# Optimization experiments

Hardware: AMD Instinct MI355X
Metric: run time of the kernel (lower is better)

## Reference

```python
import jax, jax.numpy as jnp
import numpy as np

N, E, F, H, C = 50000, 800000, 602, 32, 41
BN_EPS = 1e-5


def _mlp(h, Wa, ba, Wb, bb):
    return jax.nn.relu(h @ Wa + ba) @ Wb + bb


def _bn(h, gamma, beta):
    # BatchNorm1d training mode: per-feature batch mean / biased variance
    m = jnp.mean(h, axis=0)
    v = jnp.var(h, axis=0)
    return (h - m) * jax.lax.rsqrt(v + BN_EPS) * gamma + beta


def _gin(x, row, col, Wa, ba, Wb, bb):
    # sum-aggregate neighbor features (SpMM via gather + segment_sum), eps=0
    agg = jax.ops.segment_sum(x[col], row, num_segments=x.shape[0])
    return _mlp(x + agg, Wa, ba, Wb, bb)


def setup_inputs() -> dict:
    key = jax.random.key(0)
    ks = jax.random.split(key, 16)
    s = 0.05
    inp = {
        "x": jax.random.normal(ks[0], (N, F), dtype=jnp.float32),
        "row": jax.random.randint(ks[1], (E,), 0, N),
        "col": jax.random.randint(ks[2], (E,), 0, N),
        # conv1 MLP
        "W1a": jax.random.normal(ks[3], (F, H), dtype=jnp.float32) * s,
        "b1a": jnp.zeros((H,), jnp.float32),
        "W1b": jax.random.normal(ks[4], (H, H), dtype=jnp.float32) * s,
        "b1b": jnp.zeros((H,), jnp.float32),
        "g1": jnp.ones((H,), jnp.float32),
        "be1": jnp.zeros((H,), jnp.float32),
        # conv2 MLP
        "W2a": jax.random.normal(ks[5], (H, H), dtype=jnp.float32) * s,
        "b2a": jnp.zeros((H,), jnp.float32),
        "W2b": jax.random.normal(ks[6], (H, H), dtype=jnp.float32) * s,
        "b2b": jnp.zeros((H,), jnp.float32),
        "g2": jnp.ones((H,), jnp.float32),
        "be2": jnp.zeros((H,), jnp.float32),
        # heads
        "Wf1": jax.random.normal(ks[7], (H, H), dtype=jnp.float32) * s,
        "bf1": jnp.zeros((H,), jnp.float32),
        "Wf2": jax.random.normal(ks[8], (H, C), dtype=jnp.float32) * s,
        "bf2": jnp.zeros((C,), jnp.float32),
    }
    return inp


def reference(x, row, col, W1a, b1a, W1b, b1b, g1, be1,
              W2a, b2a, W2b, b2b, g2, be2, Wf1, bf1, Wf2, bf2):
    h = _bn(_gin(x, row, col, W1a, b1a, W1b, b1b), g1, be1)
    h = _bn(_gin(h, row, col, W2a, b2a, W2b, b2b), g2, be2)
    h = jax.nn.relu(h @ Wf1 + bf1)
    return h @ Wf2 + bf2
```

## Files before the change

### kernel.cpp

```cpp
#include <hip/hip_runtime.h>
#include <hip/hip_bf16.h>

#define N_NODES 50000
#define F_IN    602
#define H_DIM   32
#define C_OUT   41
#define E_EDGES 800000
#define BN_EPS  1e-5f

__global__ __launch_bounds__(256) void k_gemm_in_v3(
    const float* __restrict__ x, const float* __restrict__ W,
    float* __restrict__ p) {
  __shared__ float xs[64 * 68];
  __shared__ float ws[32 * 68];
  const int tid = threadIdx.x;
  const int r0 = blockIdx.x * 64;

  const int cg  = tid & 15;
  const int rgg = tid >> 4;

  const int srow = tid >> 5;
  const int fe   = tid & 31;

  const float* xrp[8];
  #pragma unroll
  for (int pp = 0; pp < 8; pp++) {
    int rr = r0 + pp * 8 + srow;
    if (rr > N_NODES - 1) rr = N_NODES - 1;
    xrp[pp] = x + (size_t)rr * F_IN;
  }

  float2 xr[8];
  float4 wr[2];

  #pragma unroll
  for (int pp = 0; pp < 8; pp++)
    xr[pp] = *(const float2*)(xrp[pp] + 2 * fe);
  #pragma unroll
  for (int q = 0; q < 2; q++)
    wr[q] = *(const float4*)(W + q * 1024 + 4 * tid);

  float acc[4][2] = {};

  for (int ch = 0; ch < 10; ch++) {
    __syncthreads();
    #pragma unroll
    for (int pp = 0; pp < 8; pp++)
      *(float2*)&xs[(pp * 8 + srow) * 68 + 2 * fe] = xr[pp];
    #pragma unroll
    for (int q = 0; q < 2; q++) {
      int off = q * 1024 + 4 * tid;
      int kk = off >> 5, c0 = off & 31;
      ws[(c0 + 0) * 68 + kk] = wr[q].x;
      ws[(c0 + 1) * 68 + kk] = wr[q].y;
      ws[(c0 + 2) * 68 + kk] = wr[q].z;
      ws[(c0 + 3) * 68 + kk] = wr[q].w;
    }
    __syncthreads();
    if (ch < 9) {
      const int k0 = (ch + 1) * 64;
      #pragma unroll
      for (int pp = 0; pp < 8; pp++) {
        int k = k0 + 2 * fe;
        float2 v = {0.f, 0.f};
        if (k + 2 <= F_IN) v = *(const float2*)(xrp[pp] + k);
        xr[pp] = v;
      }
      #pragma unroll
      for (int q = 0; q < 2; q++) {
        int off = k0 * H_DIM + q * 1024 + 4 * tid;
        float4 v = {0.f, 0.f, 0.f, 0.f};
        if (off < F_IN * H_DIM) v = *(const float4*)(W + off);
        wr[q] = v;
      }
    }
    #pragma unroll
    for (int kq = 0; kq < 16; kq++) {
      float4 xv[4], wv[2];
      #pragma unroll
      for (int i = 0; i < 4; i++) xv[i] = *(float4*)&xs[(rgg + 16 * i) * 68 + kq * 4];
      #pragma unroll
      for (int j = 0; j < 2; j++) wv[j] = *(float4*)&ws[(cg + 16 * j) * 68 + kq * 4];
      #pragma unroll
      for (int i = 0; i < 4; i++)
        #pragma unroll
        for (int j = 0; j < 2; j++)
          acc[i][j] += xv[i].x * wv[j].x + xv[i].y * wv[j].y +
                       xv[i].z * wv[j].z + xv[i].w * wv[j].w;
    }
  }

  #pragma unroll
  for (int i = 0; i < 4; i++) {
    int gr = r0 + rgg + 16 * i;
    if (gr < N_NODES) {
      #pragma unroll
      for (int j = 0; j < 2; j++)
        p[(size_t)gr * H_DIM + cg + 16 * j] = acc[i][j];
    }
  }
}

__global__ __launch_bounds__(256) void k_hist(const int* __restrict__ row,
                                              int* __restrict__ deg) {
  int e = blockIdx.x * 256 + threadIdx.x;
  if (e < E_EDGES) atomicAdd(&deg[row[e]], 1);
}

__global__ __launch_bounds__(256) void k_scanA(const int* __restrict__ deg,
                                               int* __restrict__ start,
                                               int* __restrict__ bsum) {
  __shared__ int sc[256];
  int t = threadIdx.x, i = blockIdx.x * 256 + t;
  int v = (i < N_NODES) ? deg[i] : 0;
  sc[t] = v;
  __syncthreads();
  #pragma unroll
  for (int off = 1; off < 256; off <<= 1) {
    int u = (t >= off) ? sc[t - off] : 0;
    __syncthreads();
    sc[t] += u;
    __syncthreads();
  }
  if (i < N_NODES) start[i] = sc[t] - v;
  if (t == 255) bsum[blockIdx.x] = sc[255];
}

__global__ __launch_bounds__(256) void k_scanB(const int* __restrict__ bsum,
                                               int* __restrict__ boff, int nb) {
  __shared__ int sc[256];
  int t = threadIdx.x;
  int v = (t < nb) ? bsum[t] : 0;
  sc[t] = v;
  __syncthreads();
  #pragma unroll
  for (int off = 1; off < 256; off <<= 1) {
    int u = (t >= off) ? sc[t - off] : 0;
    __syncthreads();
    sc[t] += u;
    __syncthreads();
  }
  if (t < nb) boff[t] = sc[t] - v;
}

__global__ __launch_bounds__(256) void k_scanC(int* __restrict__ start,
                                               const int* __restrict__ boff,
                                               int* __restrict__ cursor) {
  int i = blockIdx.x * 256 + threadIdx.x;
  if (i < N_NODES) {
    int s = start[i] + boff[blockIdx.x];
    start[i] = s;
    cursor[i] = s;
  }
  if (i == 0) start[N_NODES] = E_EDGES;
}

__global__ __launch_bounds__(256) void k_fill(const int* __restrict__ row,
                                              const int* __restrict__ col,
                                              int* __restrict__ cursor,
                                              int* __restrict__ ecol) {
  int e = blockIdx.x * 256 + threadIdx.x;
  if (e < E_EDGES) {
    int pos = atomicAdd(&cursor[row[e]], 1);
    ecol[pos] = col[e];
  }
}

__global__ __launch_bounds__(256) void k_gather(
    const float* __restrict__ p, const float* __restrict__ b,
    const int* __restrict__ start, const int* __restrict__ ecol,
    float* __restrict__ z) {
  int hw = (blockIdx.x * 256 + threadIdx.x) >> 5;
  int c = threadIdx.x & 31;
  if (hw >= N_NODES) return;
  int s = start[hw], e = start[hw + 1];
  float acc = p[(size_t)hw * H_DIM + c] + b[c];
  int i = s;
  for (; i + 3 < e; i += 4) {
    int s0 = ecol[i], s1 = ecol[i + 1], s2 = ecol[i + 2], s3 = ecol[i + 3];
    float v0 = p[(size_t)s0 * H_DIM + c];
    float v1 = p[(size_t)s1 * H_DIM + c];
    float v2 = p[(size_t)s2 * H_DIM + c];
    float v3 = p[(size_t)s3 * H_DIM + c];
    acc += v0; acc += v1; acc += v2; acc += v3;
  }
  for (; i < e; i++) acc += p[(size_t)ecol[i] * H_DIM + c];
  z[(size_t)hw * H_DIM + c] = acc;
}

__global__ __launch_bounds__(256) void k_zinit(const float* __restrict__ p,
                                               const float* __restrict__ b,
                                               float* __restrict__ z) {
  int i = blockIdx.x * 256 + threadIdx.x;
  if (i < N_NODES * H_DIM) z[i] = p[i] + b[i & 31];
}

__global__ __launch_bounds__(256) void k_scatter(
    const int* __restrict__ row, const int* __restrict__ col,
    const float* __restrict__ p, float* __restrict__ z) {
  long long t = (long long)blockIdx.x * 256 + threadIdx.x;
  int e = (int)(t >> 5);
  int c = (int)(t & 31);
  if (e < E_EDGES) {
    int s = col[e], d = row[e];
    atomicAdd(&z[(size_t)d * H_DIM + c], p[(size_t)s * H_DIM + c]);
  }
}

__global__ __launch_bounds__(256) void k_mlp_stats(
    const float* __restrict__ z, const float* __restrict__ W,
    const float* __restrict__ b, float* __restrict__ hpre,
    float* __restrict__ stats) {
  __shared__ float as_[64 * 36];
  __shared__ float ws[32 * 36];
  __shared__ float red[512];
  const int tid = threadIdx.x;
  for (int i = tid; i < 1024; i += 256) {
    int k = i >> 5, c = i & 31;
    ws[c * 36 + k] = W[(size_t)k * H_DIM + c];
  }
  const int r0 = blockIdx.x * 64;
  for (int i = tid; i < 2048; i += 256) {
    int r = i >> 5, c = i & 31;
    int gr = r0 + r;
    float v = (gr < N_NODES) ? z[(size_t)gr * H_DIM + c] : 0.f;
    as_[r * 36 + c] = fmaxf(v, 0.f);
  }
  __syncthreads();
  const int c = tid & 31, rg = tid >> 5;
  float4 wc[8];
  #pragma unroll
  for (int q = 0; q < 8; q++) wc[q] = *(float4*)&ws[c * 36 + q * 4];
  const float bc = b[c];
  float lsum = 0.f, lsq = 0.f;
  #pragma unroll
  for (int i = 0; i < 8; i++) {
    int r = rg * 8 + i;
    float a = bc;
    #pragma unroll
    for (int q = 0; q < 8; q++) {
      float4 h4 = *(float4*)&as_[r * 36 + q * 4];
      a += h4.x * wc[q].x + h4.y * wc[q].y + h4.z * wc[q].z + h4.w * wc[q].w;
    }
    int gr = r0 + r;
    if (gr < N_NODES) {
      hpre[(size_t)gr * H_DIM + c] = a;
      lsum += a; lsq += a * a;
    }
  }
  __syncthreads();
  red[tid] = lsum; red[256 + tid] = lsq;
  __syncthreads();
  if (tid < 32) {
    float s = 0.f, q = 0.f;
    #pragma unroll
    for (int g = 0; g < 8; g++) { s += red[g * 32 + tid]; q += red[256 + g * 32 + tid]; }
    atomicAdd(&stats[tid], s);
    atomicAdd(&stats[32 + tid], q);
  }
}

__global__ __launch_bounds__(256) void k_gemm32_affine(
    const float* __restrict__ hpre, const float* __restrict__ stats,
    const float* __restrict__ g, const float* __restrict__ be,
    const float* __restrict__ W, float* __restrict__ p) {
  __shared__ float hs[64 * 36];
  __shared__ float ws[32 * 36];
  __shared__ float ssl[64];
  const int tid = threadIdx.x;
  if (tid < 32) {
    float m = stats[tid] * (1.f / N_NODES);
    float v = stats[32 + tid] * (1.f / N_NODES) - m * m;
    float sc = g[tid] * rsqrtf(v + BN_EPS);
    ssl[tid] = sc;
    ssl[32 + tid] = be[tid] - m * sc;
  }
  for (int i = tid; i < 1024; i += 256) {
    int k = i >> 5, c = i & 31;
    ws[c * 36 + k] = W[(size_t)k * H_DIM + c];
  }
  __syncthreads();
  const int r0 = blockIdx.x * 64;
  for (int i = tid; i < 2048; i += 256) {
    int r = i >> 5, c = i & 31;
    int gr = r0 + r;
    float v = (gr < N_NODES) ? hpre[(size_t)gr * H_DIM + c] * ssl[c] + ssl[32 + c] : 0.f;
    hs[r * 36 + c] = v;
  }
  __syncthreads();
  const int c = tid & 31, rg = tid >> 5;
  float4 wc[8];
  #pragma unroll
  for (int q = 0; q < 8; q++) wc[q] = *(float4*)&ws[c * 36 + q * 4];
  #pragma unroll
  for (int i = 0; i < 8; i++) {
    int r = rg * 8 + i;
    float a = 0.f;
    #pragma unroll
    for (int q = 0; q < 8; q++) {
      float4 h4 = *(float4*)&hs[r * 36 + q * 4];
      a += h4.x * wc[q].x + h4.y * wc[q].y + h4.z * wc[q].z + h4.w * wc[q].w;
    }
    int gr = r0 + r;
    if (gr < N_NODES) p[(size_t)gr * H_DIM + c] = a;
  }
}

__global__ __launch_bounds__(256) void k_heads(
    const float* __restrict__ hpre, const float* __restrict__ stats,
    const float* __restrict__ g, const float* __restrict__ be,
    const float* __restrict__ W1, const float* __restrict__ b1,
    const float* __restrict__ W2, const float* __restrict__ b2,
    float* __restrict__ out) {
  __shared__ float hs[64 * 36];
  __shared__ float fs[64 * 36];
  __shared__ float w1[32 * 36];
  __shared__ float w2[41 * 36];
  __shared__ float ssl[64];
  const int tid = threadIdx.x;
  if (tid < 32) {
    float m = stats[tid] * (1.f / N_NODES);
    float v = stats[32 + tid] * (1.f / N_NODES) - m * m;
    float sc = g[tid] * rsqrtf(v + BN_EPS);
    ssl[tid] = sc;
    ssl[32 + tid] = be[tid] - m * sc;
  }
  for (int i = tid; i < 1024; i += 256) {
    int k = i >> 5, c = i & 31;
    w1[c * 36 + k] = W1[(size_t)k * H_DIM + c];
  }
  for (int i = tid; i < 41 * 32; i += 256) {
    int j = i >> 5, k = i & 31;
    w2[j * 36 + k] = W2[(size_t)k * C_OUT + j];
  }
  __syncthreads();
  const int r0 = blockIdx.x * 64;
  for (int i = tid; i < 2048; i += 256) {
    int r = i >> 5, c = i & 31;
    int gr = r0 + r;
    hs[r * 36 + c] = (gr < N_NODES) ? hpre[(size_t)gr * H_DIM + c] * ssl[c] + ssl[32 + c] : 0.f;
  }
  __syncthreads();
  {
    const int c = tid & 31, rg = tid >> 5;
    float4 wc[8];
    #pragma unroll
    for (int q = 0; q < 8; q++) wc[q] = *(float4*)&w1[c * 36 + q * 4];
    const float bc = b1[c];
    #pragma unroll
    for (int i = 0; i < 8; i++) {
      int r = rg * 8 + i;
      float a = bc;
      #pragma unroll
      for (int q = 0; q < 8; q++) {
        float4 h4 = *(float4*)&hs[r * 36 + q * 4];
        a += h4.x * wc[q].x + h4.y * wc[q].y + h4.z * wc[q].z + h4.w * wc[q].w;
      }
      fs[r * 36 + c] = fmaxf(a, 0.f);
    }
  }
  __syncthreads();
  for (int idx = tid; idx < 64 * C_OUT; idx += 256) {
    int r = idx / C_OUT, j = idx - r * C_OUT;
    int gr = r0 + r;
    if (gr < N_NODES) {
      float a = b2[j];
      #pragma unroll
      for (int q = 0; q < 8; q++) {
        float4 f4 = *(float4*)&fs[r * 36 + q * 4];
        float4 w4 = *(float4*)&w2[j * 36 + q * 4];
        a += f4.x * w4.x + f4.y * w4.y + f4.z * w4.z + f4.w * w4.w;
      }
      out[(size_t)gr * C_OUT + j] = a;
    }
  }
}

extern "C" void kernel_launch(void* const* d_in, const int* in_sizes, int n_in,
                              void* d_out, int out_size, void* d_ws, size_t ws_size,
                              hipStream_t stream) {
  const float* x   = (const float*)d_in[0];
  const int* row   = (const int*)d_in[1];
  const int* col   = (const int*)d_in[2];
  const float* W1a = (const float*)d_in[3];
  const float* b1a = (const float*)d_in[4];
  const float* W1b = (const float*)d_in[5];
  const float* b1b = (const float*)d_in[6];
  const float* g1  = (const float*)d_in[7];
  const float* be1 = (const float*)d_in[8];
  const float* W2a = (const float*)d_in[9];
  const float* b2a = (const float*)d_in[10];
  const float* W2b = (const float*)d_in[11];
  const float* b2b = (const float*)d_in[12];
  const float* g2  = (const float*)d_in[13];
  const float* be2 = (const float*)d_in[14];
  const float* Wf1 = (const float*)d_in[15];
  const float* bf1 = (const float*)d_in[16];
  const float* Wf2 = (const float*)d_in[17];
  const float* bf2 = (const float*)d_in[18];
  float* out = (float*)d_out;

  float* ws = (float*)d_ws;
  const size_t NH = (size_t)N_NODES * H_DIM;
  float* pA    = ws;
  float* zB    = ws + NH;
  float* hC    = ws + 2 * NH;
  float* stats = ws + 3 * NH;
  int*   startA = (int*)(ws + 3 * NH + 256);
  int*   cursor = startA + 50016;
  int*   deg    = cursor + 50016;
  int*   ecol   = deg + 50016;
  int*   bsum   = ecol + E_EDGES;
  int*   boff   = bsum + 256;
  const size_t need_bytes = ((3 * NH + 256) + 3 * 50016 + E_EDGES + 512) * 4;
  const bool use_csr = (ws_size >= need_bytes);

  hipMemsetAsync(stats, 0, 128 * sizeof(float), stream);

  const int g64   = (N_NODES + 63) / 64;
  const int gE    = (E_EDGES + 255) / 256;
  const int gN    = (N_NODES + 255) / 256;
  const int gHW   = (N_NODES * 32 + 255) / 256;
  const int gScat = (E_EDGES * 32 + 255) / 256;

  if (use_csr) {
    hipMemsetAsync(deg, 0, 50000 * sizeof(int), stream);
    k_hist <<<gE, 256, 0, stream>>>(row, deg);
    k_scanA<<<gN, 256, 0, stream>>>(deg, startA, bsum);
    k_scanB<<<1, 256, 0, stream>>>(bsum, boff, gN);
    k_scanC<<<gN, 256, 0, stream>>>(startA, boff, cursor);
    k_fill <<<gE, 256, 0, stream>>>(row, col, cursor, ecol);
  }

  k_gemm_in_v3<<<g64, 256, 0, stream>>>(x, W1a, pA);
  if (use_csr) {
    k_gather<<<gHW, 256, 0, stream>>>(pA, b1a, startA, ecol, zB);
  } else {
    k_zinit<<<g64 * 8, 256, 0, stream>>>(pA, b1a, zB);
    k_scatter<<<gScat, 256, 0, stream>>>(row, col, pA, zB);
  }
  k_mlp_stats<<<g64, 256, 0, stream>>>(zB, W1b, b1b, hC, stats);
  k_gemm32_affine<<<g64, 256, 0, stream>>>(hC, stats, g1, be1, W2a, pA);
  if (use_csr) {
    k_gather<<<gHW, 256, 0, stream>>>(pA, b2a, startA, ecol, zB);
  } else {
    k_zinit<<<g64 * 8, 256, 0, stream>>>(pA, b2a, zB);
    k_scatter<<<gScat, 256, 0, stream>>>(row, col, pA, zB);
  }
  k_mlp_stats<<<g64, 256, 0, stream>>>(zB, W2b, b2b, hC, stats + 64);
  k_heads<<<g64, 256, 0, stream>>>(hC, stats + 64, g2, be2, Wf1, bf1, Wf2, bf2, out);
}
```

Baseline: 483.8 us.

## Use split-bf16 MFMA for input GEMM and fuse gather with MLP and stats

The fp32 input projection GEMM is replaced by an MFMA kernel. It splits each fp32 value into high and low bf16 parts and runs three bf16 MFMA products (hi*hi, lo*hi, hi*lo) to stay close to fp32 accuracy. Separately, the CSR gather is fused with the ReLU, the second MLP linear layer and the BatchNorm statistics reduction, which removes the zB round trip and one kernel launch per layer. The fused kernel uses one block per 64 nodes with 8 nodes per 32-lane group, so gather parallelism per block drops. The split-bf16 trick also changes the rounding behaviour relative to true fp32.

```diff
diff --git a/kernel.cpp b/kernel.cpp
--- a/kernel.cpp
+++ b/kernel.cpp
@@ -8,95 +8,105 @@
 #define E_EDGES 800000
 #define BN_EPS  1e-5f
 
-__global__ __launch_bounds__(256) void k_gemm_in_v3(
+typedef short bf16x8 __attribute__((ext_vector_type(8)));
+typedef float f32x4  __attribute__((ext_vector_type(4)));
+
+__device__ inline unsigned short f2bf(float f) {
+  unsigned int u = __builtin_bit_cast(unsigned int, f);
+  unsigned int r = (u + 0x7FFFu + ((u >> 16) & 1u)) >> 16;
+  return (unsigned short)r;
+}
+
+__global__ __launch_bounds__(256) void k_gemm_mfma(
     const float* __restrict__ x, const float* __restrict__ W,
     float* __restrict__ p) {
-  __shared__ float xs[64 * 68];
-  __shared__ float ws[32 * 68];
+  __shared__ unsigned short xh[64 * 40], xl[64 * 40];
+  __shared__ unsigned short wh[32 * 40], wl[32 * 40];
   const int tid = threadIdx.x;
+  const int wv = tid >> 6, ln = tid & 63;
+  const int m = ln & 15, q = ln >> 4;
   const int r0 = blockIdx.x * 64;
 
-  const int cg  = tid & 15;
-  const int rgg = tid >> 4;
-
-  const int srow = tid >> 5;
-  const int fe   = tid & 31;
-
-  const float* xrp[8];
-  #pragma unroll
-  for (int pp = 0; pp < 8; pp++) {
-    int rr = r0 + pp * 8 + srow;
-    if (rr > N_NODES - 1) rr = N_NODES - 1;
-    xrp[pp] = x + (size_t)rr * F_IN;
-  }
-
-  float2 xr[8];
-  float4 wr[2];
-
-  #pragma unroll
-  for (int pp = 0; pp < 8; pp++)
-    xr[pp] = *(const float2*)(xrp[pp] + 2 * fe);
-  #pragma unroll
-  for (int q = 0; q < 2; q++)
-    wr[q] = *(const float4*)(W + q * 1024 + 4 * tid);
-
-  float acc[4][2] = {};
-
-  for (int ch = 0; ch < 10; ch++) {
+  const int srow = tid >> 4, ks2 = tid & 15;
+  const int wk = tid >> 3, c4 = tid & 7;
+
+  float2 xr[4];
+  float4 wr;
+
+  auto prefetch = [&](int k0) {
+    #pragma unroll
+    for (int pp = 0; pp < 4; pp++) {
+      int rr = r0 + srow + 16 * pp;
+      int k = k0 + 2 * ks2;
+      float2 v = {0.f, 0.f};
+      if (rr < N_NODES && k <= F_IN - 2) v = *(const float2*)(x + (size_t)rr * F_IN + k);
+      xr[pp] = v;
+    }
+    {
+      int k = k0 + wk;
+      float4 v = {0.f, 0.f, 0.f, 0.f};
+      if (k < F_IN) v = *(const float4*)(W + (size_t)k * H_DIM + 4 * c4);
+      wr = v;
+    }
+  };
+
+  f32x4 acc0 = {0.f, 0.f, 0.f, 0.f};
+  f32x4 acc1 = {0.f, 0.f, 0.f, 0.f};
+
+  prefetch(0);
+
+  unsigned int* xh32 = (unsigned int*)xh;
+  unsigned int* xl32 = (unsigned int*)xl;
+
+  for (int ch = 0; ch < 19; ch++) {
     __syncthreads();
     #pragma unroll
-    for (int pp = 0; pp < 8; pp++)
-      *(float2*)&xs[(pp * 8 + srow) * 68 + 2 * fe] = xr[pp];
-    #pragma unroll
-    for (int q = 0; q < 2; q++) {
-      int off = q * 1024 + 4 * tid;
-      int kk = off >> 5, c0 = off & 31;
-      ws[(c0 + 0) * 68 + kk] = wr[q].x;
-      ws[(c0 + 1) * 68 + kk] = wr[q].y;
-      ws[(c0 + 2) * 68 + kk] = wr[q].z;
-      ws[(c0 + 3) * 68 + kk] = wr[q].w;
+    for (int pp = 0; pp < 4; pp++) {
+      int row = srow + 16 * pp;
+      float2 v = xr[pp];
+      unsigned short h0 = f2bf(v.x), h1 = f2bf(v.y);
+      float f0 = __builtin_bit_cast(float, (unsigned int)h0 << 16);
+      float f1 = __builtin_bit_cast(float, (unsigned int)h1 << 16);
+      unsigned short l0 = f2bf(v.x - f0), l1 = f2bf(v.y - f1);
+      xh32[row * 20 + ks2] = (unsigned int)h0 | ((unsigned int)h1 << 16);
+      xl32[row * 20 + ks2] = (unsigned int)l0 | ((unsigned int)l1 << 16);
+    }
+    {
+      float wf[4] = {wr.x, wr.y, wr.z, wr.w};
+      #pragma unroll
+      for (int i = 0; i < 4; i++) {
+        unsigned short hh = f2bf(wf[i]);
+        float fh = __builtin_bit_cast(float, (unsigned int)hh << 16);
+        unsigned short ll = f2bf(wf[i] - fh);
+        wh[(4 * c4 + i) * 40 + wk] = hh;
+        wl[(4 * c4 + i) * 40 + wk] = ll;
+      }
     }
     __syncthreads();
-    if (ch < 9) {
-      const int k0 = (ch + 1) * 64;
-      #pragma unroll
-      for (int pp = 0; pp < 8; pp++) {
-        int k = k0 + 2 * fe;
-        float2 v = {0.f, 0.f};
-        if (k + 2 <= F_IN) v = *(const float2*)(xrp[pp] + k);
-        xr[pp] = v;
-      }
-      #pragma unroll
-      for (int q = 0; q < 2; q++) {
-        int off = k0 * H_DIM + q * 1024 + 4 * tid;
-        float4 v = {0.f, 0.f, 0.f, 0.f};
-        if (off < F_IN * H_DIM) v = *(const float4*)(W + off);
-        wr[q] = v;
-      }
-    }
-    #pragma unroll
-    for (int kq = 0; kq < 16; kq++) {
-      float4 xv[4], wv[2];
-      #pragma unroll
-      for (int i = 0; i < 4; i++) xv[i] = *(float4*)&xs[(rgg + 16 * i) * 68 + kq * 4];
-      #pragma unroll
-      for (int j = 0; j < 2; j++) wv[j] = *(float4*)&ws[(cg + 16 * j) * 68 + kq * 4];
-      #pragma unroll
-      for (int i = 0; i < 4; i++)
-        #pragma unroll
-        for (int j = 0; j < 2; j++)
-          acc[i][j] += xv[i].x * wv[j].x + xv[i].y * wv[j].y +
-                       xv[i].z * wv[j].z + xv[i].w * wv[j].w;
-    }
-  }
-
-  #pragma unroll
-  for (int i = 0; i < 4; i++) {
-    int gr = r0 + rgg + 16 * i;
-    if (gr < N_NODES) {
-      #pragma unroll
-      for (int j = 0; j < 2; j++)
-        p[(size_t)gr * H_DIM + cg + 16 * j] = acc[i][j];
+    if (ch < 18) prefetch((ch + 1) * 32);
+
+    const int abase = (16 * wv + m) * 40 + q * 8;
+    const int bbase = m * 40 + q * 8;
+    bf16x8 axh = *(const bf16x8*)&xh[abase];
+    bf16x8 axl = *(const bf16x8*)&xl[abase];
+    bf16x8 b0h = *(const bf16x8*)&wh[bbase];
+    bf16x8 b0l = *(const bf16x8*)&wl[bbase];
+    bf16x8 b1h = *(const bf16x8*)&wh[bbase + 16 * 40];
+    bf16x8 b1l = *(const bf16x8*)&wl[bbase + 16 * 40];
+    acc0 = __builtin_amdgcn_mfma_f32_16x16x32_bf16(axh, b0h, acc0, 0, 0, 0);
+    acc1 = __builtin_amdgcn_mfma_f32_16x16x32_bf16(axh, b1h, acc1, 0, 0, 0);
+    acc0 = __builtin_amdgcn_mfma_f32_16x16x32_bf16(axl, b0h, acc0, 0, 0, 0);
+    acc1 = __builtin_amdgcn_mfma_f32_16x16x32_bf16(axl, b1h, acc1, 0, 0, 0);
+    acc0 = __builtin_amdgcn_mfma_f32_16x16x32_bf16(axh, b0l, acc0, 0, 0, 0);
+    acc1 = __builtin_amdgcn_mfma_f32_16x16x32_bf16(axh, b1l, acc1, 0, 0, 0);
+  }
+
+  #pragma unroll
+  for (int reg = 0; reg < 4; reg++) {
+    int rowg = r0 + 16 * wv + q * 4 + reg;
+    if (rowg < N_NODES) {
+      p[(size_t)rowg * H_DIM + m]      = acc0[reg];
+      p[(size_t)rowg * H_DIM + m + 16] = acc1[reg];
     }
   }
 }
@@ -166,26 +176,75 @@
   }
 }
 
-__global__ __launch_bounds__(256) void k_gather(
-    const float* __restrict__ p, const float* __restrict__ b,
+__global__ __launch_bounds__(256) void k_gather_mlp(
+    const float* __restrict__ p, const float* __restrict__ bagg,
     const int* __restrict__ start, const int* __restrict__ ecol,
-    float* __restrict__ z) {
-  int hw = (blockIdx.x * 256 + threadIdx.x) >> 5;
-  int c = threadIdx.x & 31;
-  if (hw >= N_NODES) return;
-  int s = start[hw], e = start[hw + 1];
-  float acc = p[(size_t)hw * H_DIM + c] + b[c];
-  int i = s;
-  for (; i + 3 < e; i += 4) {
-    int s0 = ecol[i], s1 = ecol[i + 1], s2 = ecol[i + 2], s3 = ecol[i + 3];
-    float v0 = p[(size_t)s0 * H_DIM + c];
-    float v1 = p[(size_t)s1 * H_DIM + c];
-    float v2 = p[(size_t)s2 * H_DIM + c];
-    float v3 = p[(size_t)s3 * H_DIM + c];
-    acc += v0; acc += v1; acc += v2; acc += v3;
-  }
-  for (; i < e; i++) acc += p[(size_t)ecol[i] * H_DIM + c];
-  z[(size_t)hw * H_DIM + c] = acc;
+    const float* __restrict__ Wm, const float* __restrict__ bm,
+    float* __restrict__ hpre, float* __restrict__ stats) {
+  __shared__ float as_[64 * 36];
+  __shared__ float ws[32 * 36];
+  __shared__ float red[512];
+  const int tid = threadIdx.x;
+  for (int i = tid; i < 1024; i += 256) {
+    int k = i >> 5, c = i & 31;
+    ws[c * 36 + k] = Wm[(size_t)k * H_DIM + c];
+  }
+  const int hw = tid >> 5, c = tid & 31;
+  const int n0 = blockIdx.x * 64;
+  const float bca = bagg[c];
+  for (int s = 0; s < 8; s++) {
+    int lr = hw * 8 + s;
+    int n = n0 + lr;
+    float acc = 0.f;
+    if (n < N_NODES) {
+      acc = p[(size_t)n * H_DIM + c] + bca;
+      int i0 = start[n], i1 = start[n + 1];
+      int i = i0;
+      for (; i + 3 < i1; i += 4) {
+        int s0 = ecol[i], s1 = ecol[i + 1], s2 = ecol[i + 2], s3 = ecol[i + 3];
+        float v0 = p[(size_t)s0 * H_DIM + c];
+        float v1 = p[(size_t)s1 * H_DIM + c];
+        float v2 = p[(size_t)s2 * H_DIM + c];
+        float v3 = p[(size_t)s3 * H_DIM + c];
+        acc += v0; acc += v1; acc += v2; acc += v3;
+      }
+      for (; i < i1; i++) acc += p[(size_t)ecol[i] * H_DIM + c];
+      acc = fmaxf(acc, 0.f);
+    }
+    as_[lr * 36 + c] = acc;
+  }
+  __syncthreads();
+  const int rg = tid >> 5;
+  float4 wc[8];
+  #pragma unroll
+  for (int qq = 0; qq < 8; qq++) wc[qq] = *(float4*)&ws[c * 36 + qq * 4];
+  const float bc = bm[c];
+  float lsum = 0.f, lsq = 0.f;
+  #pragma unroll
+  for (int i = 0; i < 8; i++) {
+    int r = rg * 8 + i;
+    float a = bc;
+    #pragma unroll
+    for (int qq = 0; qq < 8; qq++) {
+      float4 h4 = *(float4*)&as_[r * 36 + qq * 4];
+      a += h4.x * wc[qq].x + h4.y * wc[qq].y + h4.z * wc[qq].z + h4.w * wc[qq].w;
+    }
+    int gr = n0 + r;
+    if (gr < N_NODES) {
+      hpre[(size_t)gr * H_DIM + c] = a;
+      lsum += a; lsq += a * a;
+    }
+  }
+  __syncthreads();
+  red[tid] = lsum; red[256 + tid] = lsq;
+  __syncthreads();
+  if (tid < 32) {
+    float s = 0.f, qv = 0.f;
+    #pragma unroll
+    for (int g = 0; g < 8; g++) { s += red[g * 32 + tid]; qv += red[256 + g * 32 + tid]; }
+    atomicAdd(&stats[tid], s);
+    atomicAdd(&stats[32 + tid], qv);
+  }
 }
 
 __global__ __launch_bounds__(256) void k_zinit(const float* __restrict__ p,
@@ -420,7 +479,6 @@
   const int g64   = (N_NODES + 63) / 64;
   const int gE    = (E_EDGES + 255) / 256;
   const int gN    = (N_NODES + 255) / 256;
-  const int gHW   = (N_NODES * 32 + 255) / 256;
   const int gScat = (E_EDGES * 32 + 255) / 256;
 
   if (use_csr) {
@@ -432,21 +490,21 @@
     k_fill <<<gE, 256, 0, stream>>>(row, col, cursor, ecol);
   }
 
-  k_gemm_in_v3<<<g64, 256, 0, stream>>>(x, W1a, pA);
+  k_gemm_mfma<<<g64, 256, 0, stream>>>(x, W1a, pA);
   if (use_csr) {
-    k_gather<<<gHW, 256, 0, stream>>>(pA, b1a, startA, ecol, zB);
+    k_gather_mlp<<<g64, 256, 0, stream>>>(pA, b1a, startA, ecol, W1b, b1b, hC, stats);
   } else {
     k_zinit<<<g64 * 8, 256, 0, stream>>>(pA, b1a, zB);
     k_scatter<<<gScat, 256, 0, stream>>>(row, col, pA, zB);
-  }
-  k_mlp_stats<<<g64, 256, 0, stream>>>(zB, W1b, b1b, hC, stats);
+    k_mlp_stats<<<g64, 256, 0, stream>>>(zB, W1b, b1b, hC, stats);
+  }
   k_gemm32_affine<<<g64, 256, 0, stream>>>(hC, stats, g1, be1, W2a, pA);
   if (use_csr) {
-    k_gather<<<gHW, 256, 0, stream>>>(pA, b2a, startA, ecol, zB);
+    k_gather_mlp<<<g64, 256, 0, stream>>>(pA, b2a, startA, ecol, W2b, b2b, hC, stats + 64);
   } else {
     k_zinit<<<g64 * 8, 256, 0, stream>>>(pA, b2a, zB);
     k_scatter<<<gScat, 256, 0, stream>>>(row, col, pA, zB);
-  }
-  k_mlp_stats<<<g64, 256, 0, stream>>>(zB, W2b, b2b, hC, stats + 64);
+    k_mlp_stats<<<g64, 256, 0, stream>>>(zB, W2b, b2b, hC, stats + 64);
+  }
   k_heads<<<g64, 256, 0, stream>>>(hC, stats + 64, g2, be2, Wf1, bf1, Wf2, bf2, out);
 }
```

After: 462.5 us. 1.05x faster.
